# Optimization experiments

Measured on AMD Instinct MI355X. Metric: run time of the kernel, lower is better.

The kernel has to match this reference:

```python
import jax, jax.numpy as jnp
from jax import lax
import numpy as np

MAX_REGIONS = 4          # static cap on connected components per volume
BIG = np.int32(2 ** 30)  # 'infinity' label for background in CCL
INF = jnp.float32(1e10)  # 'infinity' squared distance for EDT


def setup_inputs() -> dict:
    key = jax.random.key(0)
    B, D, H, W = 2, 96, 96, 96
    zz, yy, xx = np.meshgrid(np.arange(D), np.arange(H), np.arange(W), indexing='ij')

    def sphere(c, r):
        return (zz - c[0]) ** 2 + (yy - c[1]) ** 2 + (xx - c[2]) ** 2 <= r * r

    vols = []
    for b in range(B):  # 3 disjoint components per volume (realistic lesion GT)
        m = sphere((24 + 4 * b, 24, 24), 10) | sphere((70, 60, 30 + 6 * b), 12) | sphere((48, 72, 72), 9)
        vols.append(m)
    y = jnp.asarray(np.stack(vols)[:, None].astype(np.int32))          # (B,1,D,H,W)
    x = jax.random.normal(key, (B, 1, D, H, W), dtype=jnp.float32)     # logits
    return {"x": x, "y": y}


def _ccl(mask):
    """26-connected components (skimage/cucim default) via min-label propagation.
    Returns comp: int32 labels 1..K in raster order of first voxel (0 = bg), and K."""
    idx = jnp.arange(mask.size, dtype=jnp.int32).reshape(mask.shape)
    lab0 = jnp.where(mask, idx, BIG)

    def step(c):
        lab, _ = c
        pooled = lax.reduce_window(lab, BIG, lax.min, (3, 3, 3), (1, 1, 1), 'SAME')
        new = jnp.where(mask, pooled, BIG)
        return (new, jnp.any(new != lab))

    lab, _ = lax.while_loop(lambda c: c[1], step, (lab0, jnp.bool_(True)))
    uniq = jnp.unique(lab, size=MAX_REGIONS + 1, fill_value=BIG)  # sorted roots, padded
    K = jnp.sum(uniq < BIG).astype(jnp.int32)
    comp = jnp.searchsorted(uniq, lab.ravel()).reshape(lab.shape).astype(jnp.int32) + 1
    comp = jnp.where(mask, comp, 0)
    return comp, K


def _edt_1d(f, axis):
    """Exact 1D squared-EDT pass: out[p] = min_q (p-q)^2 + f[q]."""
    f2 = jnp.moveaxis(f, axis, 0)
    sh = f2.shape
    L = sh[0]
    f2 = f2.reshape(L, -1)
    q = jnp.arange(L, dtype=f.dtype)
    d2 = (q[:, None] - q[None, :]) ** 2                 # (L, L)
    out = jnp.min(d2[:, :, None] + f2[None, :, :], axis=1)  # (L, M)
    return jnp.moveaxis(out.reshape(sh), 0, axis)


def _edt_sq(f0):
    for ax in range(3):
        f0 = _edt_1d(f0, ax)
    return f0  # exact squared Euclidean distance to the zero set


def _voronoi(comp):
    """region_map[v] = label of nearest component (ties -> smallest label),
    mirroring the torch strict-< update loop over region labels."""
    def one(r):
        f0 = jnp.where(comp == r, jnp.float32(0.0), INF)
        return _edt_sq(f0)

    dists = lax.map(one, jnp.arange(1, MAX_REGIONS + 1, dtype=jnp.int32))  # (R,D,H,W)
    return jnp.argmin(dists, axis=0).astype(jnp.int32) + 1  # first-occurrence tie-break


def _per_volume(xb, yb):
    mask = yb > 0
    comp, K = _ccl(mask)              # multi_label: component labels 1..K
    region = _voronoi(comp)           # Voronoi regionization, labels 1..MAX_REGIONS
    seg = (region - 1).ravel()
    xs = jax.nn.sigmoid(xb).ravel()
    yl = comp.astype(jnp.float32).ravel()  # dice uses label VALUES, as in torch
    inter = jax.ops.segment_sum(xs * yl, seg, num_segments=MAX_REGIONS)
    sx = jax.ops.segment_sum(xs, seg, num_segments=MAX_REGIONS)
    sy = jax.ops.segment_sum(yl, seg, num_segments=MAX_REGIONS)
    valid = jnp.arange(MAX_REGIONS) < K
    denom = jnp.where(valid, sx + sy, jnp.float32(1.0))
    dice_r = jnp.where(valid, 2.0 * inter / denom, jnp.float32(0.0))
    mean_dice = jnp.sum(dice_r) / jnp.maximum(K, 1).astype(jnp.float32)
    return jnp.where(K == 0, jnp.float32(1.0), 1.0 - mean_dice)


def reference(x, y):
    # x: (B,1,D,H,W) logits; y: (B,1,D,H,W) int binary GT
    losses = lax.map(lambda t: _per_volume(t[0], t[1]), (x[:, 0], y[:, 0]))
    return jnp.mean(losses)
```

## Files before the change

kernel.cpp:

```cpp
#include <hip/hip_runtime.h>
#include <math.h>

#define W3 96
#define HW 9216
#define DHW 884736
#define NB 2
#define BIGL (1<<30)
#define INF10 1.0e10f
#define CAND_CAP 8192

#define A_ROOTCNT 0
#define A_ROOTS   2
#define A_CANDCNT 18
#define A_SUMS    28
#define A_TOTAL   64

__global__ void k_local(const int* __restrict__ y, int* __restrict__ lab,
                        int* __restrict__ acc, int* __restrict__ cand) {
    __shared__ int l[512];
    __shared__ int anyflag;
    int blk = blockIdx.x, t = threadIdx.x;
    if (t == 0) anyflag = 0;
    int b = blk / 1728, tb = blk - b * 1728;
    int tz = tb / 72, rr2 = tb - tz * 72, ty = rr2 / 3, tx = rr2 - ty * 3;
    int d0 = tz * 4, h0 = ty * 4, w0 = tx * 32;
    const int* yb = y + b * DHW;
    int* lb = lab + b * DHW;
    int e0 = t, e1 = t + 256;
    int dz0 = e0 >> 7, dy0 = (e0 >> 5) & 3, dx0 = e0 & 31;
    int dz1 = e1 >> 7, dy1 = (e1 >> 5) & 3, dx1 = e1 & 31;
    int g0 = (d0 + dz0) * HW + (h0 + dy0) * W3 + (w0 + dx0);
    int g1 = (d0 + dz1) * HW + (h0 + dy1) * W3 + (w0 + dx1);
    int m0 = yb[g0] > 0, m1 = yb[g1] > 0;
    l[e0] = m0 ? e0 : 0x7FFF0000;
    l[e1] = m1 ? e1 : 0x7FFF0000;
    __syncthreads();
    if (m0 | m1) anyflag = 1;
    __syncthreads();
    if (!anyflag) { lb[g0] = BIGL; lb[g1] = BIGL; return; }

    for (int it = 0; it < 7; it++) {
        int n0, n1;
        n0 = l[e0]; n1 = l[e1];
        if (m0) { if (dx0 > 0) n0 = min(n0, l[e0 - 1]);  if (dx0 < 31) n0 = min(n0, l[e0 + 1]); }
        if (m1) { if (dx1 > 0) n1 = min(n1, l[e1 - 1]);  if (dx1 < 31) n1 = min(n1, l[e1 + 1]); }
        __syncthreads();
        if (m0) l[e0] = n0;  if (m1) l[e1] = n1;
        __syncthreads();
        n0 = l[e0]; n1 = l[e1];
        if (m0) { if (dy0 > 0) n0 = min(n0, l[e0 - 32]); if (dy0 < 3) n0 = min(n0, l[e0 + 32]); }
        if (m1) { if (dy1 > 0) n1 = min(n1, l[e1 - 32]); if (dy1 < 3) n1 = min(n1, l[e1 + 32]); }
        __syncthreads();
        if (m0) l[e0] = n0;  if (m1) l[e1] = n1;
        __syncthreads();
        n0 = l[e0]; n1 = l[e1];
        if (m0) { if (dz0 > 0) n0 = min(n0, l[e0 - 128]); if (dz0 < 3) n0 = min(n0, l[e0 + 128]); }
        if (m1) { if (dz1 > 0) n1 = min(n1, l[e1 - 128]); if (dz1 < 3) n1 = min(n1, l[e1 + 128]); }
        __syncthreads();
        if (m0) l[e0] = n0;  if (m1) l[e1] = n1;
        __syncthreads();
        n0 = m0 ? l[l[e0]] : 0;  n1 = m1 ? l[l[e1]] : 0;
        __syncthreads();
        if (m0) l[e0] = n0;  if (m1) l[e1] = n1;
        __syncthreads();
    }
    if (m0) {
        int r = l[e0]; while (l[r] != r) r = l[r];
        lb[g0] = (d0 + (r >> 7)) * HW + (h0 + ((r >> 5) & 3)) * W3 + (w0 + (r & 31));
        if (r == e0) { int c = atomicAdd(&acc[A_CANDCNT + b], 1);
                       if (c < CAND_CAP) cand[b * CAND_CAP + c] = g0; }
    } else lb[g0] = BIGL;
    if (m1) {
        int r = l[e1]; while (l[r] != r) r = l[r];
        lb[g1] = (d0 + (r >> 7)) * HW + (h0 + ((r >> 5) & 3)) * W3 + (w0 + (r & 31));
        if (r == e1) { int c = atomicAdd(&acc[A_CANDCNT + b], 1);
                       if (c < CAND_CAP) cand[b * CAND_CAP + c] = g1; }
    } else lb[g1] = BIGL;
}

__device__ __forceinline__ int ufind(int* __restrict__ lb, int v) {
    int p = lb[v];
    if (p == v) return p;
    int root = p;
    while (true) { int pp = lb[root]; if (pp == root) break; root = pp; }
    if (root < p) atomicMin(&lb[v], root);
    return root;
}

__device__ void unite(int* __restrict__ lb, int a, int b) {
    while (true) {
        a = ufind(lb, a); b = ufind(lb, b);
        if (a == b) return;
        int mn = min(a, b), mx = max(a, b);
        int old = atomicMin(&lb[mx], mn);
        if (old == mx) return;
        a = old; b = mn;
    }
}

__constant__ int c_offs[13][3] = {
    {-1,-1,-1},{-1,-1,0},{-1,-1,1},
    {-1, 0,-1},{-1, 0,0},{-1, 0,1},
    {-1, 1,-1},{-1, 1,0},{-1, 1,1},
    { 0,-1,-1},{ 0,-1,0},{ 0,-1,1},
    { 0, 0,-1}};

__global__ void k_bmerge(const int* __restrict__ y, int* __restrict__ lab) {
    int i = blockIdx.x * blockDim.x + threadIdx.x;
    if (i >= NB * DHW) return;
    int b = i / DHW, v = i - b * DHW;
    int d = v / HW; int rem = v - d * HW; int h = rem / W3; int w = rem - h * W3;
    int fz = ((d & 3) == 0), fy = ((h & 3) == 0), fx = ((w & 31) == 0);
    if (!(fz | fy | fx)) return;
    if (y[i] <= 0) return;
    const int* yb = y + b * DHW;
    int* lb = lab + b * DHW;
    #pragma unroll
    for (int k = 0; k < 13; k++) {
        int oz = c_offs[k][0], oy = c_offs[k][1], ox = c_offs[k][2];
        int cross = (fz && oz < 0) || (fy && oy < 0) || (fx && ox < 0);
        if (!cross) continue;
        int dd = d + oz, hh = h + oy, ww = w + ox;
        if ((unsigned)dd >= W3 || (unsigned)hh >= W3 || (unsigned)ww >= W3) continue;
        int u = dd * HW + hh * W3 + ww;
        if (yb[u] > 0) unite(lb, v, u);
    }
}

__global__ void k_collect(const int* __restrict__ lab, int* __restrict__ acc,
                          const int* __restrict__ cand) {
    int b = blockIdx.x;
    int t = threadIdx.x;
    int cnt = acc[A_CANDCNT + b]; if (cnt > CAND_CAP) cnt = CAND_CAP;
    const int* lb = lab + (size_t)b * DHW;
    for (int i = t; i < cnt; i += 256) {
        int g = cand[b * CAND_CAP + i];
        if (lb[g] == g) {
            int c = atomicAdd(&acc[A_ROOTCNT + b], 1);
            if (c < 8) acc[A_ROOTS + b * 8 + c] = g;
        }
    }
}

__device__ __forceinline__ int gfind(const int* __restrict__ lb, int t) {
    while (true) { int p = lb[t]; if (p == t) break; t = p; }
    return t;
}

__device__ __forceinline__ int rankc2(int t, const int rt[8], int n) {
    int c = 1;
    #pragma unroll
    for (int p = 0; p < 8; p++) c += (p < n && rt[p] < t) ? 1 : 0;
    return c;
}

__device__ __forceinline__ int wrmin(int v) {
    v = min(v, __shfl_xor(v, 32, 64)); v = min(v, __shfl_xor(v, 16, 64));
    v = min(v, __shfl_xor(v, 8, 64));  v = min(v, __shfl_xor(v, 4, 64));
    v = min(v, __shfl_xor(v, 2, 64));  v = min(v, __shfl_xor(v, 1, 64));
    return v;
}
__device__ __forceinline__ int wrmax(int v) {
    v = max(v, __shfl_xor(v, 32, 64)); v = max(v, __shfl_xor(v, 16, 64));
    v = max(v, __shfl_xor(v, 8, 64));  v = max(v, __shfl_xor(v, 4, 64));
    v = max(v, __shfl_xor(v, 2, 64));  v = max(v, __shfl_xor(v, 1, 64));
    return v;
}

__global__ __launch_bounds__(384) void k_pedtD(const int* __restrict__ lab,
                                               const int* __restrict__ acc,
                                               float* __restrict__ out) {
    __shared__ float A[96 * 101];
    __shared__ int qlo, qhi;
    int blk = blockIdx.x;
    int b = blk / 384, r = blk % 384;
    int h = r >> 2, d0 = (r & 3) * 24;
    const int* lb = lab + (size_t)b * DHW;
    int t = threadIdx.x;
    if (t == 0) { qlo = 127; qhi = -1; }
    int n = acc[A_ROOTCNT + b]; if (n > 8) n = 8;
    int rt[8];
    #pragma unroll
    for (int p = 0; p < 8; p++) rt[p] = acc[A_ROOTS + b * 8 + p];
    __syncthreads();
    size_t vbase = (size_t)b * DHW;
    int w2 = t % 96, tq = t / 96;
    int myLo = 127, myHi = -1;
    #pragma unroll
    for (int m = 0; m < 24; m++) {
        int dd = tq + 4 * m;
        int tv = lb[dd * HW + h * W3 + w2];
        float val = INF10;
        if (tv != BIGL) {
            val = 0.125f * (float)rankc2(gfind(lb, tv), rt, n);
            myLo = min(myLo, dd); myHi = max(myHi, dd);
        }
        A[dd * 101 + w2] = (float)(dd * dd) + val;
    }
    myLo = wrmin(myLo); myHi = wrmax(myHi);
    if ((t & 63) == 0) { atomicMin(&qlo, myLo); atomicMax(&qhi, myHi); }
    __syncthreads();
    int w = t % 96, dg = t / 96;
    int dbase = d0 + dg * 6;
    int lo = qlo, hi = qhi;
    if (hi < 0) {
        #pragma unroll
        for (int k = 0; k < 6; k++)
            out[vbase + (size_t)(dbase + k) * HW + h * W3 + w] = INF10;
        return;
    }
    float best[6], pk[6];
    #pragma unroll
    for (int k = 0; k < 6; k++) { best[k] = 3.9e37f; pk[k] = (float)(dbase + k); }
    float m2q = -2.0f * (float)lo;
    for (int q = lo; q <= hi; q++) {
        float val = A[q * 101 + w];
        #pragma unroll
        for (int k = 0; k < 6; k++)
            best[k] = fminf(best[k], fmaf(pk[k], m2q, val));
        m2q -= 2.0f;
    }
    #pragma unroll
    for (int k = 0; k < 6; k++)
        out[vbase + (size_t)(dbase + k) * HW + h * W3 + w] = best[k] + pk[k] * pk[k];
}

__device__ __forceinline__ float wred(float v) {
    v += __shfl_xor(v, 32, 64);
    v += __shfl_xor(v, 16, 64);
    v += __shfl_xor(v, 8, 64);
    v += __shfl_xor(v, 4, 64);
    v += __shfl_xor(v, 2, 64);
    v += __shfl_xor(v, 1, 64);
    return v;
}

__global__ __launch_bounds__(384) void k_pedtHW_acc(const float* __restrict__ fin,
                                                    const float* __restrict__ x,
                                                    int* __restrict__ acc) {
    __shared__ float A[96 * 101];
    __shared__ float Bf[24 * 101];
    __shared__ int hlo, hhi, wlo, whi;
    __shared__ float red[6][12];
    int blk = blockIdx.x;
    int b = blk / 384, r = blk % 384;
    int d = r >> 2, h0 = (r & 3) * 24;
    size_t sbase = (size_t)b * DHW + (size_t)d * HW;
    int t = threadIdx.x;
    if (t == 0) { hlo = 127; hhi = -1; wlo = 127; whi = -1; }
    __syncthreads();
    int w2 = t % 96, tq = t / 96;
    int myLo = 127, myHi = -1, myWLo = 127, myWHi = -1;
    #pragma unroll
    for (int m = 0; m < 24; m++) {
        int hh = tq + 4 * m;
        float val = fin[sbase + hh * W3 + w2];
        if (val < 1.0e9f) {
            myLo = min(myLo, hh); myHi = max(myHi, hh);
            myWLo = w2; myWHi = w2;
        }
        A[hh * 101 + w2] = (float)(hh * hh) + val;
    }
    if (myWHi < 0) myWLo = 127;
    myLo = wrmin(myLo); myHi = wrmax(myHi);
    myWLo = wrmin(myWLo); myWHi = wrmax(myWHi);
    if ((t & 63) == 0) {
        atomicMin(&hlo, myLo); atomicMax(&hhi, myHi);
        atomicMin(&wlo, myWLo); atomicMax(&whi, myWHi);
    }
    __syncthreads();
    {
        int w = t % 96, hg = t / 96;
        int hb = h0 + hg * 6;
        int lo = hlo, hi = hhi;
        float fw2 = (float)(w * w);
        if (hi < 0) {
            #pragma unroll
            for (int k = 0; k < 6; k++) Bf[(hg * 6 + k) * 101 + w] = INF10;
        } else {
            float best[6], pk[6];
            #pragma unroll
            for (int k = 0; k < 6; k++) { best[k] = 3.9e37f; pk[k] = (float)(hb + k); }
            float m2q = -2.0f * (float)lo;
            for (int q = lo; q <= hi; q++) {
                float val = A[q * 101 + w];
                #pragma unroll
                for (int k = 0; k < 6; k++)
                    best[k] = fminf(best[k], fmaf(pk[k], m2q, val));
                m2q -= 2.0f;
            }
            #pragma unroll
            for (int k = 0; k < 6; k++)
                Bf[(hg * 6 + k) * 101 + w] = best[k] + pk[k] * pk[k] + fw2;
        }
    }
    __syncthreads();
    {
        int rr = t % 24, cg = t / 24;
        int wb = cg * 6;
        int lo = wlo, hi = whi;
        if (hi < 0) {
            #pragma unroll
            for (int k = 0; k < 6; k++) A[rr * 101 + wb + k] = INF10;
        } else {
            float best[6], pk[6];
            #pragma unroll
            for (int k = 0; k < 6; k++) { best[k] = 3.9e37f; pk[k] = (float)(wb + k); }
            float m2q = -2.0f * (float)lo;
            for (int q = lo; q <= hi; q++) {
                float val = Bf[rr * 101 + q];
                #pragma unroll
                for (int k = 0; k < 6; k++)
                    best[k] = fminf(best[k], fmaf(pk[k], m2q, val));
                m2q -= 2.0f;
            }
            #pragma unroll
            for (int k = 0; k < 6; k++) A[rr * 101 + wb + k] = best[k] + pk[k] * pk[k];
        }
    }
    __syncthreads();
    float aA[4] = {0,0,0,0}, aM[4] = {0,0,0,0}, aC[4] = {0,0,0,0};
    size_t qbase = sbase + (size_t)h0 * W3;
    #pragma unroll
    for (int m = 0; m < 6; m++) {
        int e = t + 384 * m;
        int rr = e / 96, wv2 = e - rr * 96;
        float key = A[rr * 101 + wv2];
        int key8 = (int)(key * 8.0f);
        int seg = (key8 & 7) - 1;
        seg = (seg < 0) ? 0 : ((seg > 3) ? 3 : seg);
        int c = (key8 < 8) ? (seg + 1) : 0;
        float xs = 1.0f / (1.0f + __expf(-x[qbase + e]));
        #pragma unroll
        for (int s = 0; s < 4; s++) {
            aA[s] += (seg == s) ? xs : 0.0f;
            aM[s] += (c == s + 1) ? xs : 0.0f;
            aC[s] += (c == s + 1) ? 1.0f : 0.0f;
        }
    }
    #pragma unroll
    for (int s = 0; s < 4; s++) { aA[s] = wred(aA[s]); aM[s] = wred(aM[s]); aC[s] = wred(aC[s]); }
    int lane = t & 63, wv = t >> 6;
    if (lane == 0) {
        #pragma unroll
        for (int s = 0; s < 4; s++) {
            red[wv][s] = aA[s]; red[wv][4 + s] = aM[s]; red[wv][8 + s] = aC[s];
        }
    }
    __syncthreads();
    if (t < 12) {
        float v = red[0][t] + red[1][t] + red[2][t] + red[3][t] + red[4][t] + red[5][t];
        atomicAdd((float*)&acc[A_SUMS + b * 12 + t], v);
    }
}

__global__ void k_loss(const int* __restrict__ acc, float* __restrict__ out) {
    if (threadIdx.x == 0 && blockIdx.x == 0) {
        const float* sums = (const float*)&acc[A_SUMS];
        float total = 0.0f;
        for (int b = 0; b < NB; b++) {
            int n = acc[A_ROOTCNT + b];
            int K = (n > 5) ? 5 : n;
            float s = 0.0f;
            for (int r = 0; r < 4; r++) {
                if (r < K) {
                    float A = sums[b * 12 + r];
                    float M = sums[b * 12 + 4 + r];
                    float C = sums[b * 12 + 8 + r];
                    float inter = (float)(r + 1) * M;
                    float sy = (float)(r + 1) * C;
                    s += 2.0f * inter / (A + sy);
                }
            }
            float Kf = (float)(K > 0 ? K : 1);
            total += (K == 0) ? 1.0f : (1.0f - s / Kf);
        }
        out[0] = total / (float)NB;
    }
}

extern "C" void kernel_launch(void* const* d_in, const int* in_sizes, int n_in,
                              void* d_out, int out_size, void* d_ws, size_t ws_size,
                              hipStream_t stream) {
    const float* x = (const float*)d_in[0];
    const int*   y = (const int*)d_in[1];
    float* out = (float*)d_out;

    char* ws = (char*)d_ws;
    int*   acc  = (int*)ws;
    int*   cand = (int*)(ws + 1024);
    int*   lab  = (int*)(ws + 1024 + CAND_CAP * NB * 4);
    float* kB   = (float*)((char*)lab + (size_t)NB * DHW * 4);

    dim3 blk(256);
    dim3 g1((NB * DHW) / 256);
    dim3 gl(NB * 1728);
    dim3 gq(NB * 96 * 4);
    dim3 b384(384);

    hipMemsetAsync(acc, 0, 256, stream);
    k_local<<<gl, blk, 0, stream>>>(y, lab, acc, cand);
    k_bmerge<<<g1, blk, 0, stream>>>(y, lab);
    k_collect<<<NB, blk, 0, stream>>>(lab, acc, cand);
    k_pedtD<<<gq, b384, 0, stream>>>(lab, acc, kB);
    k_pedtHW_acc<<<gq, b384, 0, stream>>>(kB, x, acc);
    k_loss<<<1, 64, 0, stream>>>(acc, out);
}
```

Before: 168.5 us.

## Fuse CCL and EDT pipeline into one cooperative persistent kernel

```diff
diff --git a/kernel.cpp b/kernel.cpp
--- a/kernel.cpp
+++ b/kernel.cpp
@@ -1,5 +1,8 @@
 #include <hip/hip_runtime.h>
+#include <hip/hip_cooperative_groups.h>
 #include <math.h>
+
+namespace cg = cooperative_groups;
 
 #define W3 96
 #define HW 9216
@@ -8,6 +11,9 @@
 #define BIGL (1<<30)
 #define INF10 1.0e10f
 #define CAND_CAP 8192
+#define NTHR 384
+#define NJOBS 768
+#define NCU 256
 
 #define A_ROOTCNT 0
 #define A_ROOTS   2
@@ -15,68 +21,18 @@
 #define A_SUMS    28
 #define A_TOTAL   64
 
-__global__ void k_local(const int* __restrict__ y, int* __restrict__ lab,
-                        int* __restrict__ acc, int* __restrict__ cand) {
-    __shared__ int l[512];
-    __shared__ int anyflag;
-    int blk = blockIdx.x, t = threadIdx.x;
-    if (t == 0) anyflag = 0;
-    int b = blk / 1728, tb = blk - b * 1728;
-    int tz = tb / 72, rr2 = tb - tz * 72, ty = rr2 / 3, tx = rr2 - ty * 3;
-    int d0 = tz * 4, h0 = ty * 4, w0 = tx * 32;
-    const int* yb = y + b * DHW;
-    int* lb = lab + b * DHW;
-    int e0 = t, e1 = t + 256;
-    int dz0 = e0 >> 7, dy0 = (e0 >> 5) & 3, dx0 = e0 & 31;
-    int dz1 = e1 >> 7, dy1 = (e1 >> 5) & 3, dx1 = e1 & 31;
-    int g0 = (d0 + dz0) * HW + (h0 + dy0) * W3 + (w0 + dx0);
-    int g1 = (d0 + dz1) * HW + (h0 + dy1) * W3 + (w0 + dx1);
-    int m0 = yb[g0] > 0, m1 = yb[g1] > 0;
-    l[e0] = m0 ? e0 : 0x7FFF0000;
-    l[e1] = m1 ? e1 : 0x7FFF0000;
-    __syncthreads();
-    if (m0 | m1) anyflag = 1;
-    __syncthreads();
-    if (!anyflag) { lb[g0] = BIGL; lb[g1] = BIGL; return; }
-
-    for (int it = 0; it < 7; it++) {
-        int n0, n1;
-        n0 = l[e0]; n1 = l[e1];
-        if (m0) { if (dx0 > 0) n0 = min(n0, l[e0 - 1]);  if (dx0 < 31) n0 = min(n0, l[e0 + 1]); }
-        if (m1) { if (dx1 > 0) n1 = min(n1, l[e1 - 1]);  if (dx1 < 31) n1 = min(n1, l[e1 + 1]); }
-        __syncthreads();
-        if (m0) l[e0] = n0;  if (m1) l[e1] = n1;
-        __syncthreads();
-        n0 = l[e0]; n1 = l[e1];
-        if (m0) { if (dy0 > 0) n0 = min(n0, l[e0 - 32]); if (dy0 < 3) n0 = min(n0, l[e0 + 32]); }
-        if (m1) { if (dy1 > 0) n1 = min(n1, l[e1 - 32]); if (dy1 < 3) n1 = min(n1, l[e1 + 32]); }
-        __syncthreads();
-        if (m0) l[e0] = n0;  if (m1) l[e1] = n1;
-        __syncthreads();
-        n0 = l[e0]; n1 = l[e1];
-        if (m0) { if (dz0 > 0) n0 = min(n0, l[e0 - 128]); if (dz0 < 3) n0 = min(n0, l[e0 + 128]); }
-        if (m1) { if (dz1 > 0) n1 = min(n1, l[e1 - 128]); if (dz1 < 3) n1 = min(n1, l[e1 + 128]); }
-        __syncthreads();
-        if (m0) l[e0] = n0;  if (m1) l[e1] = n1;
-        __syncthreads();
-        n0 = m0 ? l[l[e0]] : 0;  n1 = m1 ? l[l[e1]] : 0;
-        __syncthreads();
-        if (m0) l[e0] = n0;  if (m1) l[e1] = n1;
-        __syncthreads();
-    }
-    if (m0) {
-        int r = l[e0]; while (l[r] != r) r = l[r];
-        lb[g0] = (d0 + (r >> 7)) * HW + (h0 + ((r >> 5) & 3)) * W3 + (w0 + (r & 31));
-        if (r == e0) { int c = atomicAdd(&acc[A_CANDCNT + b], 1);
-                       if (c < CAND_CAP) cand[b * CAND_CAP + c] = g0; }
-    } else lb[g0] = BIGL;
-    if (m1) {
-        int r = l[e1]; while (l[r] != r) r = l[r];
-        lb[g1] = (d0 + (r >> 7)) * HW + (h0 + ((r >> 5) & 3)) * W3 + (w0 + (r & 31));
-        if (r == e1) { int c = atomicAdd(&acc[A_CANDCNT + b], 1);
-                       if (c < CAND_CAP) cand[b * CAND_CAP + c] = g1; }
-    } else lb[g1] = BIGL;
-}
+__constant__ int c_offs[13][3] = {
+    {-1,-1,-1},{-1,-1,0},{-1,-1,1},
+    {-1, 0,-1},{-1, 0,0},{-1, 0,1},
+    {-1, 1,-1},{-1, 1,0},{-1, 1,1},
+    { 0,-1,-1},{ 0,-1,0},{ 0,-1,1},
+    { 0, 0,-1}};
+
+struct SP1 { int l[512]; int flag; };
+struct SP4 { float A[96 * 101]; int qlo, qhi; };
+struct SP5 { float A[96 * 101]; float Bf[24 * 101]; float red[6][12];
+             int hlo, hhi, wlo, whi; };
+union SMem { SP1 p1; SP4 p4; SP5 p5; };
 
 __device__ __forceinline__ int ufind(int* __restrict__ lb, int v) {
     int p = lb[v];
@@ -98,50 +54,6 @@
     }
 }
 
-__constant__ int c_offs[13][3] = {
-    {-1,-1,-1},{-1,-1,0},{-1,-1,1},
-    {-1, 0,-1},{-1, 0,0},{-1, 0,1},
-    {-1, 1,-1},{-1, 1,0},{-1, 1,1},
-    { 0,-1,-1},{ 0,-1,0},{ 0,-1,1},
-    { 0, 0,-1}};
-
-__global__ void k_bmerge(const int* __restrict__ y, int* __restrict__ lab) {
-    int i = blockIdx.x * blockDim.x + threadIdx.x;
-    if (i >= NB * DHW) return;
-    int b = i / DHW, v = i - b * DHW;
-    int d = v / HW; int rem = v - d * HW; int h = rem / W3; int w = rem - h * W3;
-    int fz = ((d & 3) == 0), fy = ((h & 3) == 0), fx = ((w & 31) == 0);
-    if (!(fz | fy | fx)) return;
-    if (y[i] <= 0) return;
-    const int* yb = y + b * DHW;
-    int* lb = lab + b * DHW;
-    #pragma unroll
-    for (int k = 0; k < 13; k++) {
-        int oz = c_offs[k][0], oy = c_offs[k][1], ox = c_offs[k][2];
-        int cross = (fz && oz < 0) || (fy && oy < 0) || (fx && ox < 0);
-        if (!cross) continue;
-        int dd = d + oz, hh = h + oy, ww = w + ox;
-        if ((unsigned)dd >= W3 || (unsigned)hh >= W3 || (unsigned)ww >= W3) continue;
-        int u = dd * HW + hh * W3 + ww;
-        if (yb[u] > 0) unite(lb, v, u);
-    }
-}
-
-__global__ void k_collect(const int* __restrict__ lab, int* __restrict__ acc,
-                          const int* __restrict__ cand) {
-    int b = blockIdx.x;
-    int t = threadIdx.x;
-    int cnt = acc[A_CANDCNT + b]; if (cnt > CAND_CAP) cnt = CAND_CAP;
-    const int* lb = lab + (size_t)b * DHW;
-    for (int i = t; i < cnt; i += 256) {
-        int g = cand[b * CAND_CAP + i];
-        if (lb[g] == g) {
-            int c = atomicAdd(&acc[A_ROOTCNT + b], 1);
-            if (c < 8) acc[A_ROOTS + b * 8 + c] = g;
-        }
-    }
-}
-
 __device__ __forceinline__ int gfind(const int* __restrict__ lb, int t) {
     while (true) { int p = lb[t]; if (p == t) break; t = p; }
     return t;
@@ -166,124 +78,161 @@
     v = max(v, __shfl_xor(v, 2, 64));  v = max(v, __shfl_xor(v, 1, 64));
     return v;
 }
-
-__global__ __launch_bounds__(384) void k_pedtD(const int* __restrict__ lab,
-                                               const int* __restrict__ acc,
-                                               float* __restrict__ out) {
-    __shared__ float A[96 * 101];
-    __shared__ int qlo, qhi;
-    int blk = blockIdx.x;
-    int b = blk / 384, r = blk % 384;
-    int h = r >> 2, d0 = (r & 3) * 24;
+__device__ __forceinline__ float wred(float v) {
+    v += __shfl_xor(v, 32, 64); v += __shfl_xor(v, 16, 64);
+    v += __shfl_xor(v, 8, 64);  v += __shfl_xor(v, 4, 64);
+    v += __shfl_xor(v, 2, 64);  v += __shfl_xor(v, 1, 64);
+    return v;
+}
+
+__device__ void phase1(const int* __restrict__ y, int* __restrict__ lab,
+                       int* __restrict__ acc, int* __restrict__ cand,
+                       SP1* sm, int blk, int nblk, int t) {
+    for (int tile = blk; tile < NB * 1728; tile += nblk) {
+        int b = tile / 1728, tb = tile - b * 1728;
+        int tz = tb / 72, rr2 = tb - tz * 72, ty = rr2 / 3, tx = rr2 - ty * 3;
+        int d0 = tz * 4, h0 = ty * 4, w0 = tx * 32;
+        const int* yb = y + b * DHW;
+        int* lb = lab + b * DHW;
+        if (t == 0) sm->flag = 0;
+        __syncthreads();
+        int e0 = t, e1 = t + NTHR;
+        int has1 = (e1 < 512);
+        int dz0 = e0 >> 7, dy0 = (e0 >> 5) & 3, dx0 = e0 & 31;
+        int dz1 = e1 >> 7, dy1 = (e1 >> 5) & 3, dx1 = e1 & 31;
+        int g0 = (d0 + dz0) * HW + (h0 + dy0) * W3 + (w0 + dx0);
+        int g1 = (d0 + dz1) * HW + (h0 + dy1) * W3 + (w0 + dx1);
+        int m0 = yb[g0] > 0;
+        int m1 = has1 ? (yb[g1] > 0) : 0;
+        sm->l[e0] = m0 ? e0 : 0x7FFF0000;
+        if (has1) sm->l[e1] = m1 ? e1 : 0x7FFF0000;
+        if (m0 | m1) sm->flag = 1;
+        __syncthreads();
+        if (sm->flag) {
+            int* l = sm->l;
+            for (int it = 0; it < 7; it++) {
+                int n0 = 0, n1 = 0;
+                if (m0) { n0 = l[e0]; if (dx0 > 0) n0 = min(n0, l[e0 - 1]);  if (dx0 < 31) n0 = min(n0, l[e0 + 1]); }
+                if (m1) { n1 = l[e1]; if (dx1 > 0) n1 = min(n1, l[e1 - 1]);  if (dx1 < 31) n1 = min(n1, l[e1 + 1]); }
+                __syncthreads();
+                if (m0) l[e0] = n0;  if (m1) l[e1] = n1;
+                __syncthreads();
+                if (m0) { n0 = l[e0]; if (dy0 > 0) n0 = min(n0, l[e0 - 32]); if (dy0 < 3) n0 = min(n0, l[e0 + 32]); }
+                if (m1) { n1 = l[e1]; if (dy1 > 0) n1 = min(n1, l[e1 - 32]); if (dy1 < 3) n1 = min(n1, l[e1 + 32]); }
+                __syncthreads();
+                if (m0) l[e0] = n0;  if (m1) l[e1] = n1;
+                __syncthreads();
+                if (m0) { n0 = l[e0]; if (dz0 > 0) n0 = min(n0, l[e0 - 128]); if (dz0 < 3) n0 = min(n0, l[e0 + 128]); }
+                if (m1) { n1 = l[e1]; if (dz1 > 0) n1 = min(n1, l[e1 - 128]); if (dz1 < 3) n1 = min(n1, l[e1 + 128]); }
+                __syncthreads();
+                if (m0) l[e0] = n0;  if (m1) l[e1] = n1;
+                __syncthreads();
+                if (m0) n0 = l[l[e0]];
+                if (m1) n1 = l[l[e1]];
+                __syncthreads();
+                if (m0) l[e0] = n0;  if (m1) l[e1] = n1;
+                __syncthreads();
+            }
+            if (m0) {
+                int r = sm->l[e0]; while (sm->l[r] != r) r = sm->l[r];
+                lb[g0] = (d0 + (r >> 7)) * HW + (h0 + ((r >> 5) & 3)) * W3 + (w0 + (r & 31));
+                if (r == e0) { int c = atomicAdd(&acc[A_CANDCNT + b], 1);
+                               if (c < CAND_CAP) cand[b * CAND_CAP + c] = g0; }
+            }
+            if (m1) {
+                int r = sm->l[e1]; while (sm->l[r] != r) r = sm->l[r];
+                lb[g1] = (d0 + (r >> 7)) * HW + (h0 + ((r >> 5) & 3)) * W3 + (w0 + (r & 31));
+                if (r == e1) { int c = atomicAdd(&acc[A_CANDCNT + b], 1);
+                               if (c < CAND_CAP) cand[b * CAND_CAP + c] = g1; }
+            }
+        }
+        __syncthreads();
+    }
+}
+
+__device__ void phase2(const int* __restrict__ y, int* __restrict__ lab,
+                       int blk, int nblk, int t) {
+    int gid = blk * NTHR + t;
+    for (int i = gid; i < NB * DHW; i += nblk * NTHR) {
+        int b = i / DHW, v = i - b * DHW;
+        int d = v / HW; int rem = v - d * HW; int h = rem / W3; int w = rem - h * W3;
+        int fz = ((d & 3) == 0), fy = ((h & 3) == 0), fx = ((w & 31) == 0);
+        if (!(fz | fy | fx)) continue;
+        if (y[i] <= 0) continue;
+        const int* yb = y + b * DHW;
+        int* lb = lab + b * DHW;
+        #pragma unroll
+        for (int k = 0; k < 13; k++) {
+            int oz = c_offs[k][0], oy = c_offs[k][1], ox = c_offs[k][2];
+            int cross = (fz && oz < 0) || (fy && oy < 0) || (fx && ox < 0);
+            if (!cross) continue;
+            int dd = d + oz, hh = h + oy, ww = w + ox;
+            if ((unsigned)dd >= W3 || (unsigned)hh >= W3 || (unsigned)ww >= W3) continue;
+            int u = dd * HW + hh * W3 + ww;
+            if (yb[u] > 0) unite(lb, v, u);
+        }
+    }
+}
+
+__device__ void phase3(const int* __restrict__ lab, int* __restrict__ acc,
+                       const int* __restrict__ cand, int blk, int t) {
+    if (blk >= NB) return;
+    int b = blk;
+    int cnt = acc[A_CANDCNT + b]; if (cnt > CAND_CAP) cnt = CAND_CAP;
     const int* lb = lab + (size_t)b * DHW;
-    int t = threadIdx.x;
-    if (t == 0) { qlo = 127; qhi = -1; }
-    int n = acc[A_ROOTCNT + b]; if (n > 8) n = 8;
-    int rt[8];
-    #pragma unroll
-    for (int p = 0; p < 8; p++) rt[p] = acc[A_ROOTS + b * 8 + p];
-    __syncthreads();
-    size_t vbase = (size_t)b * DHW;
-    int w2 = t % 96, tq = t / 96;
-    int myLo = 127, myHi = -1;
-    #pragma unroll
-    for (int m = 0; m < 24; m++) {
-        int dd = tq + 4 * m;
-        int tv = lb[dd * HW + h * W3 + w2];
-        float val = INF10;
-        if (tv != BIGL) {
-            val = 0.125f * (float)rankc2(gfind(lb, tv), rt, n);
-            myLo = min(myLo, dd); myHi = max(myHi, dd);
-        }
-        A[dd * 101 + w2] = (float)(dd * dd) + val;
-    }
-    myLo = wrmin(myLo); myHi = wrmax(myHi);
-    if ((t & 63) == 0) { atomicMin(&qlo, myLo); atomicMax(&qhi, myHi); }
-    __syncthreads();
-    int w = t % 96, dg = t / 96;
-    int dbase = d0 + dg * 6;
-    int lo = qlo, hi = qhi;
-    if (hi < 0) {
-        #pragma unroll
-        for (int k = 0; k < 6; k++)
-            out[vbase + (size_t)(dbase + k) * HW + h * W3 + w] = INF10;
-        return;
-    }
-    float best[6], pk[6];
-    #pragma unroll
-    for (int k = 0; k < 6; k++) { best[k] = 3.9e37f; pk[k] = (float)(dbase + k); }
-    float m2q = -2.0f * (float)lo;
-    for (int q = lo; q <= hi; q++) {
-        float val = A[q * 101 + w];
-        #pragma unroll
-        for (int k = 0; k < 6; k++)
-            best[k] = fminf(best[k], fmaf(pk[k], m2q, val));
-        m2q -= 2.0f;
-    }
-    #pragma unroll
-    for (int k = 0; k < 6; k++)
-        out[vbase + (size_t)(dbase + k) * HW + h * W3 + w] = best[k] + pk[k] * pk[k];
-}
-
-__device__ __forceinline__ float wred(float v) {
-    v += __shfl_xor(v, 32, 64);
-    v += __shfl_xor(v, 16, 64);
-    v += __shfl_xor(v, 8, 64);
-    v += __shfl_xor(v, 4, 64);
-    v += __shfl_xor(v, 2, 64);
-    v += __shfl_xor(v, 1, 64);
-    return v;
-}
-
-__global__ __launch_bounds__(384) void k_pedtHW_acc(const float* __restrict__ fin,
-                                                    const float* __restrict__ x,
-                                                    int* __restrict__ acc) {
-    __shared__ float A[96 * 101];
-    __shared__ float Bf[24 * 101];
-    __shared__ int hlo, hhi, wlo, whi;
-    __shared__ float red[6][12];
-    int blk = blockIdx.x;
-    int b = blk / 384, r = blk % 384;
-    int d = r >> 2, h0 = (r & 3) * 24;
-    size_t sbase = (size_t)b * DHW + (size_t)d * HW;
-    int t = threadIdx.x;
-    if (t == 0) { hlo = 127; hhi = -1; wlo = 127; whi = -1; }
-    __syncthreads();
-    int w2 = t % 96, tq = t / 96;
-    int myLo = 127, myHi = -1, myWLo = 127, myWHi = -1;
-    #pragma unroll
-    for (int m = 0; m < 24; m++) {
-        int hh = tq + 4 * m;
-        float val = fin[sbase + hh * W3 + w2];
-        if (val < 1.0e9f) {
-            myLo = min(myLo, hh); myHi = max(myHi, hh);
-            myWLo = w2; myWHi = w2;
-        }
-        A[hh * 101 + w2] = (float)(hh * hh) + val;
-    }
-    if (myWHi < 0) myWLo = 127;
-    myLo = wrmin(myLo); myHi = wrmax(myHi);
-    myWLo = wrmin(myWLo); myWHi = wrmax(myWHi);
-    if ((t & 63) == 0) {
-        atomicMin(&hlo, myLo); atomicMax(&hhi, myHi);
-        atomicMin(&wlo, myWLo); atomicMax(&whi, myWHi);
-    }
-    __syncthreads();
-    {
-        int w = t % 96, hg = t / 96;
-        int hb = h0 + hg * 6;
-        int lo = hlo, hi = hhi;
-        float fw2 = (float)(w * w);
+    for (int i = t; i < cnt; i += NTHR) {
+        int g2 = cand[b * CAND_CAP + i];
+        if (lb[g2] == g2) {
+            int c = atomicAdd(&acc[A_ROOTCNT + b], 1);
+            if (c < 8) acc[A_ROOTS + b * 8 + c] = g2;
+        }
+    }
+}
+
+__device__ void phase4(const int* __restrict__ y, const int* __restrict__ lab,
+                       const int* __restrict__ acc, float* __restrict__ kB,
+                       SP4* sm, int blk, int nblk, int t) {
+    for (int job = blk; job < NJOBS; job += nblk) {
+        int b = job / 384, r = job % 384;
+        int h = r >> 2, d0 = (r & 3) * 24;
+        const int* lb = lab + (size_t)b * DHW;
+        const int* yb = y + (size_t)b * DHW;
+        if (t == 0) { sm->qlo = 127; sm->qhi = -1; }
+        int n = acc[A_ROOTCNT + b]; if (n > 8) n = 8;
+        int rt[8];
+        #pragma unroll
+        for (int p = 0; p < 8; p++) rt[p] = acc[A_ROOTS + b * 8 + p];
+        __syncthreads();
+        size_t vbase = (size_t)b * DHW;
+        int w2 = t % 96, tq = t / 96;
+        int myLo = 127, myHi = -1;
+        #pragma unroll
+        for (int m = 0; m < 24; m++) {
+            int dd = tq + 4 * m;
+            int gi = dd * HW + h * W3 + w2;
+            float val = INF10;
+            if (yb[gi] > 0) {
+                val = 0.125f * (float)rankc2(gfind(lb, lb[gi]), rt, n);
+                myLo = min(myLo, dd); myHi = max(myHi, dd);
+            }
+            sm->A[dd * 101 + w2] = (float)(dd * dd) + val;
+        }
+        myLo = wrmin(myLo); myHi = wrmax(myHi);
+        if ((t & 63) == 0) { atomicMin(&sm->qlo, myLo); atomicMax(&sm->qhi, myHi); }
+        __syncthreads();
+        int dbase = d0 + tq * 6;
+        int lo = sm->qlo, hi = sm->qhi;
         if (hi < 0) {
             #pragma unroll
-            for (int k = 0; k < 6; k++) Bf[(hg * 6 + k) * 101 + w] = INF10;
+            for (int k = 0; k < 6; k++)
+                kB[vbase + (size_t)(dbase + k) * HW + h * W3 + w2] = INF10;
         } else {
             float best[6], pk[6];
             #pragma unroll
-            for (int k = 0; k < 6; k++) { best[k] = 3.9e37f; pk[k] = (float)(hb + k); }
+            for (int k = 0; k < 6; k++) { best[k] = 3.9e37f; pk[k] = (float)(dbase + k); }
             float m2q = -2.0f * (float)lo;
             for (int q = lo; q <= hi; q++) {
-                float val = A[q * 101 + w];
+                float val = sm->A[q * 101 + w2];
                 #pragma unroll
                 for (int k = 0; k < 6; k++)
                     best[k] = fminf(best[k], fmaf(pk[k], m2q, val));
@@ -291,92 +240,197 @@
             }
             #pragma unroll
             for (int k = 0; k < 6; k++)
-                Bf[(hg * 6 + k) * 101 + w] = best[k] + pk[k] * pk[k] + fw2;
-        }
-    }
-    __syncthreads();
-    {
-        int rr = t % 24, cg = t / 24;
-        int wb = cg * 6;
-        int lo = wlo, hi = whi;
-        if (hi < 0) {
+                kB[vbase + (size_t)(dbase + k) * HW + h * W3 + w2] = best[k] + pk[k] * pk[k];
+        }
+        __syncthreads();
+    }
+}
+
+__device__ void phase5(const float* __restrict__ kB, const float* __restrict__ x,
+                       int* __restrict__ acc, SP5* sm, int blk, int nblk, int t) {
+    for (int job = blk; job < NJOBS; job += nblk) {
+        int b = job / 384, r = job % 384;
+        int d = r >> 2, h0 = (r & 3) * 24;
+        size_t sbase = (size_t)b * DHW + (size_t)d * HW;
+        if (t == 0) { sm->hlo = 127; sm->hhi = -1; sm->wlo = 127; sm->whi = -1; }
+        __syncthreads();
+        int w2 = t % 96, tq = t / 96;
+        int myLo = 127, myHi = -1, myWLo = 127, myWHi = -1;
+        #pragma unroll
+        for (int m = 0; m < 24; m++) {
+            int hh = tq + 4 * m;
+            float val = kB[sbase + hh * W3 + w2];
+            if (val < 1.0e9f) {
+                myLo = min(myLo, hh); myHi = max(myHi, hh);
+                myWLo = w2; myWHi = w2;
+            }
+            sm->A[hh * 101 + w2] = (float)(hh * hh) + val;
+        }
+        if (myWHi < 0) myWLo = 127;
+        myLo = wrmin(myLo); myHi = wrmax(myHi);
+        myWLo = wrmin(myWLo); myWHi = wrmax(myWHi);
+        if ((t & 63) == 0) {
+            atomicMin(&sm->hlo, myLo); atomicMax(&sm->hhi, myHi);
+            atomicMin(&sm->wlo, myWLo); atomicMax(&sm->whi, myWHi);
+        }
+        __syncthreads();
+        {
+            int w = t % 96, hg = t / 96;
+            int hb = h0 + hg * 6;
+            int lo = sm->hlo, hi = sm->hhi;
+            float fw2 = (float)(w * w);
+            if (hi < 0) {
+                #pragma unroll
+                for (int k = 0; k < 6; k++) sm->Bf[(hg * 6 + k) * 101 + w] = INF10;
+            } else {
+                float best[6], pk[6];
+                #pragma unroll
+                for (int k = 0; k < 6; k++) { best[k] = 3.9e37f; pk[k] = (float)(hb + k); }
+                float m2q = -2.0f * (float)lo;
+                for (int q = lo; q <= hi; q++) {
+                    float val = sm->A[q * 101 + w];
+                    #pragma unroll
+                    for (int k = 0; k < 6; k++)
+                        best[k] = fminf(best[k], fmaf(pk[k], m2q, val));
+                    m2q -= 2.0f;
+                }
+                #pragma unroll
+                for (int k = 0; k < 6; k++)
+                    sm->Bf[(hg * 6 + k) * 101 + w] = best[k] + pk[k] * pk[k] + fw2;
+            }
+        }
+        __syncthreads();
+        {
+            int rr = t % 24, cg2 = t / 24;
+            int wb = cg2 * 6;
+            int lo = sm->wlo, hi = sm->whi;
+            if (hi < 0) {
+                #pragma unroll
+                for (int k = 0; k < 6; k++) sm->A[rr * 101 + wb + k] = INF10;
+            } else {
+                float best[6], pk[6];
+                #pragma unroll
+                for (int k = 0; k < 6; k++) { best[k] = 3.9e37f; pk[k] = (float)(wb + k); }
+                float m2q = -2.0f * (float)lo;
+                for (int q = lo; q <= hi; q++) {
+                    float val = sm->Bf[rr * 101 + q];
+                    #pragma unroll
+                    for (int k = 0; k < 6; k++)
+                        best[k] = fminf(best[k], fmaf(pk[k], m2q, val));
+                    m2q -= 2.0f;
+                }
+                #pragma unroll
+                for (int k = 0; k < 6; k++) sm->A[rr * 101 + wb + k] = best[k] + pk[k] * pk[k];
+            }
+        }
+        __syncthreads();
+        float aA[4] = {0,0,0,0}, aM[4] = {0,0,0,0}, aC[4] = {0,0,0,0};
+        size_t qbase = sbase + (size_t)h0 * W3;
+        #pragma unroll
+        for (int m = 0; m < 6; m++) {
+            int e = t + NTHR * m;
+            int rr = e / 96, wv2 = e - rr * 96;
+            float key = sm->A[rr * 101 + wv2];
+            int key8 = (int)(key * 8.0f);
+            int seg = (key8 & 7) - 1;
+            seg = (seg < 0) ? 0 : ((seg > 3) ? 3 : seg);
+            int c = (key8 < 8) ? (seg + 1) : 0;
+            float xs = 1.0f / (1.0f + __expf(-x[qbase + e]));
             #pragma unroll
-            for (int k = 0; k < 6; k++) A[rr * 101 + wb + k] = INF10;
-        } else {
-            float best[6], pk[6];
+            for (int s = 0; s < 4; s++) {
+                aA[s] += (seg == s) ? xs : 0.0f;
+                aM[s] += (c == s + 1) ? xs : 0.0f;
+                aC[s] += (c == s + 1) ? 1.0f : 0.0f;
+            }
+        }
+        #pragma unroll
+        for (int s = 0; s < 4; s++) { aA[s] = wred(aA[s]); aM[s] = wred(aM[s]); aC[s] = wred(aC[s]); }
+        int lane = t & 63, wv = t >> 6;
+        if (lane == 0) {
             #pragma unroll
-            for (int k = 0; k < 6; k++) { best[k] = 3.9e37f; pk[k] = (float)(wb + k); }
-            float m2q = -2.0f * (float)lo;
-            for (int q = lo; q <= hi; q++) {
-                float val = Bf[rr * 101 + q];
-                #pragma unroll
-                for (int k = 0; k < 6; k++)
-                    best[k] = fminf(best[k], fmaf(pk[k], m2q, val));
-                m2q -= 2.0f;
-            }
-            #pragma unroll
-            for (int k = 0; k < 6; k++) A[rr * 101 + wb + k] = best[k] + pk[k] * pk[k];
-        }
-    }
-    __syncthreads();
-    float aA[4] = {0,0,0,0}, aM[4] = {0,0,0,0}, aC[4] = {0,0,0,0};
-    size_t qbase = sbase + (size_t)h0 * W3;
-    #pragma unroll
-    for (int m = 0; m < 6; m++) {
-        int e = t + 384 * m;
-        int rr = e / 96, wv2 = e - rr * 96;
-        float key = A[rr * 101 + wv2];
-        int key8 = (int)(key * 8.0f);
-        int seg = (key8 & 7) - 1;
-        seg = (seg < 0) ? 0 : ((seg > 3) ? 3 : seg);
-        int c = (key8 < 8) ? (seg + 1) : 0;
-        float xs = 1.0f / (1.0f + __expf(-x[qbase + e]));
-        #pragma unroll
-        for (int s = 0; s < 4; s++) {
-            aA[s] += (seg == s) ? xs : 0.0f;
-            aM[s] += (c == s + 1) ? xs : 0.0f;
-            aC[s] += (c == s + 1) ? 1.0f : 0.0f;
-        }
-    }
-    #pragma unroll
-    for (int s = 0; s < 4; s++) { aA[s] = wred(aA[s]); aM[s] = wred(aM[s]); aC[s] = wred(aC[s]); }
-    int lane = t & 63, wv = t >> 6;
-    if (lane == 0) {
-        #pragma unroll
-        for (int s = 0; s < 4; s++) {
-            red[wv][s] = aA[s]; red[wv][4 + s] = aM[s]; red[wv][8 + s] = aC[s];
-        }
-    }
-    __syncthreads();
-    if (t < 12) {
-        float v = red[0][t] + red[1][t] + red[2][t] + red[3][t] + red[4][t] + red[5][t];
-        atomicAdd((float*)&acc[A_SUMS + b * 12 + t], v);
-    }
-}
-
-__global__ void k_loss(const int* __restrict__ acc, float* __restrict__ out) {
-    if (threadIdx.x == 0 && blockIdx.x == 0) {
-        const float* sums = (const float*)&acc[A_SUMS];
-        float total = 0.0f;
-        for (int b = 0; b < NB; b++) {
-            int n = acc[A_ROOTCNT + b];
-            int K = (n > 5) ? 5 : n;
-            float s = 0.0f;
-            for (int r = 0; r < 4; r++) {
-                if (r < K) {
-                    float A = sums[b * 12 + r];
-                    float M = sums[b * 12 + 4 + r];
-                    float C = sums[b * 12 + 8 + r];
-                    float inter = (float)(r + 1) * M;
-                    float sy = (float)(r + 1) * C;
-                    s += 2.0f * inter / (A + sy);
-                }
-            }
-            float Kf = (float)(K > 0 ? K : 1);
-            total += (K == 0) ? 1.0f : (1.0f - s / Kf);
-        }
-        out[0] = total / (float)NB;
-    }
+            for (int s = 0; s < 4; s++) {
+                sm->red[wv][s] = aA[s]; sm->red[wv][4 + s] = aM[s]; sm->red[wv][8 + s] = aC[s];
+            }
+        }
+        __syncthreads();
+        if (t < 12) {
+            float v = sm->red[0][t] + sm->red[1][t] + sm->red[2][t] +
+                      sm->red[3][t] + sm->red[4][t] + sm->red[5][t];
+            atomicAdd((float*)&acc[A_SUMS + b * 12 + t], v);
+        }
+        __syncthreads();
+    }
+}
+
+__device__ void lossf(const int* __restrict__ acc, float* __restrict__ out) {
+    const float* sums = (const float*)&acc[A_SUMS];
+    float total = 0.0f;
+    for (int b = 0; b < NB; b++) {
+        int n = acc[A_ROOTCNT + b];
+        int K = (n > 5) ? 5 : n;
+        float s = 0.0f;
+        for (int r = 0; r < 4; r++) {
+            if (r < K) {
+                float A = sums[b * 12 + r];
+                float M = sums[b * 12 + 4 + r];
+                float C = sums[b * 12 + 8 + r];
+                float inter = (float)(r + 1) * M;
+                float sy = (float)(r + 1) * C;
+                s += 2.0f * inter / (A + sy);
+            }
+        }
+        float Kf = (float)(K > 0 ? K : 1);
+        total += (K == 0) ? 1.0f : (1.0f - s / Kf);
+    }
+    out[0] = total / (float)NB;
+}
+
+__global__ __launch_bounds__(NTHR) void k_mega(const float* __restrict__ x,
+                                               const int* __restrict__ y,
+                                               int* acc, int* cand, int* lab,
+                                               float* kB, float* out) {
+    cg::grid_group gg = cg::this_grid();
+    __shared__ SMem sm;
+    int t = threadIdx.x, blk = blockIdx.x, nblk = gridDim.x;
+    if (blk == 0 && t < A_TOTAL) acc[t] = 0;
+    gg.sync();
+    phase1(y, lab, acc, cand, &sm.p1, blk, nblk, t);
+    gg.sync();
+    phase2(y, lab, blk, nblk, t);
+    gg.sync();
+    phase3(lab, acc, cand, blk, t);
+    gg.sync();
+    phase4(y, lab, acc, kB, &sm.p4, blk, nblk, t);
+    gg.sync();
+    phase5(kB, x, acc, &sm.p5, blk, nblk, t);
+    gg.sync();
+    if (blk == 0 && t == 0) lossf(acc, out);
+}
+
+__global__ void k_f0(int* acc) {
+    if (blockIdx.x == 0 && threadIdx.x < A_TOTAL) acc[threadIdx.x] = 0;
+}
+__global__ __launch_bounds__(NTHR) void k_f1(const int* y, int* lab, int* acc, int* cand) {
+    __shared__ SP1 sm;
+    phase1(y, lab, acc, cand, &sm, blockIdx.x, gridDim.x, threadIdx.x);
+}
+__global__ __launch_bounds__(NTHR) void k_f2(const int* y, int* lab) {
+    phase2(y, lab, blockIdx.x, gridDim.x, threadIdx.x);
+}
+__global__ __launch_bounds__(NTHR) void k_f3(const int* lab, int* acc, const int* cand) {
+    phase3(lab, acc, cand, blockIdx.x, threadIdx.x);
+}
+__global__ __launch_bounds__(NTHR) void k_f4(const int* y, const int* lab,
+                                             const int* acc, float* kB) {
+    __shared__ SP4 sm;
+    phase4(y, lab, acc, kB, &sm, blockIdx.x, gridDim.x, threadIdx.x);
+}
+__global__ __launch_bounds__(NTHR) void k_f5(const float* kB, const float* x, int* acc) {
+    __shared__ SP5 sm;
+    phase5(kB, x, acc, &sm, blockIdx.x, gridDim.x, threadIdx.x);
+}
+__global__ void k_f6(const int* acc, float* out) {
+    if (threadIdx.x == 0 && blockIdx.x == 0) lossf(acc, out);
 }
 
 extern "C" void kernel_launch(void* const* d_in, const int* in_sizes, int n_in,
@@ -392,17 +446,27 @@
     int*   lab  = (int*)(ws + 1024 + CAND_CAP * NB * 4);
     float* kB   = (float*)((char*)lab + (size_t)NB * DHW * 4);
 
-    dim3 blk(256);
-    dim3 g1((NB * DHW) / 256);
-    dim3 gl(NB * 1728);
-    dim3 gq(NB * 96 * 4);
-    dim3 b384(384);
-
-    hipMemsetAsync(acc, 0, 256, stream);
-    k_local<<<gl, blk, 0, stream>>>(y, lab, acc, cand);
-    k_bmerge<<<g1, blk, 0, stream>>>(y, lab);
-    k_collect<<<NB, blk, 0, stream>>>(lab, acc, cand);
-    k_pedtD<<<gq, b384, 0, stream>>>(lab, acc, kB);
-    k_pedtHW_acc<<<gq, b384, 0, stream>>>(kB, x, acc);
-    k_loss<<<1, 64, 0, stream>>>(acc, out);
-}
+    int maxPerCU = 0;
+    hipError_t oe = hipOccupancyMaxActiveBlocksPerMultiprocessor(&maxPerCU, k_mega, NTHR, 0);
+    bool done = false;
+    if (oe == hipSuccess && maxPerCU > 0) {
+        int nblk = maxPerCU * NCU;
+        if (nblk > NJOBS) nblk = NJOBS;
+        if (nblk >= NB) {
+            void* args[] = {(void*)&x, (void*)&y, (void*)&acc, (void*)&cand,
+                            (void*)&lab, (void*)&kB, (void*)&out};
+            if (hipLaunchCooperativeKernel((void*)k_mega, dim3(nblk), dim3(NTHR),
+                                           args, 0, stream) == hipSuccess)
+                done = true;
+        }
+    }
+    if (!done) {
+        k_f0<<<1, 64, 0, stream>>>(acc);
+        k_f1<<<NB * 1728, NTHR, 0, stream>>>(y, lab, acc, cand);
+        k_f2<<<(NB * DHW) / NTHR, NTHR, 0, stream>>>(y, lab);
+        k_f3<<<NB, NTHR, 0, stream>>>(lab, acc, cand);
+        k_f4<<<NJOBS, NTHR, 0, stream>>>(y, lab, acc, kB);
+        k_f5<<<NJOBS, NTHR, 0, stream>>>(kB, x, acc);
+        k_f6<<<1, 64, 0, stream>>>(acc, out);
+    }
+}
```

Result: slower. 244.5 us (+45.2%).
